# Kernel optimization log

Measured on AMD Instinct MI355X. Metric: run time of the kernel, lower is better.

The kernel has to match this reference:

```python
import jax, jax.numpy as jnp
import numpy as np

BATCH = 4096
IN_SIZES = [1024, 1024, 1024, 1024]
EMB = 2048  # embracement_size


def setup_inputs() -> dict:
    key = jax.random.key(0)
    keys = jax.random.split(key, 3 * len(IN_SIZES))
    inp = {}
    for i, d in enumerate(IN_SIZES):
        inp[f"x{i}"] = jax.random.normal(keys[3 * i], (BATCH, d), dtype=jnp.float32)
        # Linear params (Kaiming-ish scale)
        inp[f"W{i}"] = jax.random.normal(keys[3 * i + 1], (d, EMB), dtype=jnp.float32) / np.sqrt(d)
        inp[f"b{i}"] = jax.random.normal(keys[3 * i + 2], (EMB,), dtype=jnp.float32) * 0.01
    return inp


def _sample_indices(batch, num_feats, emb):
    # availabilities=None, selection_probabilities=None -> uniform p over modalities
    # multinomial(p, num_samples=emb, replacement=True) == categorical over log p
    logits = jnp.zeros((batch, num_feats), dtype=jnp.float32)  # uniform
    k = jax.random.key(42)
    # shape (emb, batch) broadcasts against logits batch shape (batch,)
    idx = jax.random.categorical(k, logits, axis=-1, shape=(emb, batch))
    return idx.T  # [batch, emb]


def reference(x0, W0, b0, x1, W1, b1, x2, W2, b2, x3, W3, b3):
    xs = [x0, x1, x2, x3]
    Ws = [W0, W1, W2, W3]
    bs = [b0, b1, b2, b3]
    # docking: Linear + ReLU per modality -> [batch, EMB, num_feats]
    dock = jnp.stack([jax.nn.relu(x @ W + b) for x, W, b in zip(xs, Ws, bs)], axis=-1)
    B, E, F = dock.shape
    idx = _sample_indices(B, F, E)  # [B, E] int32
    # gather along modality axis (replaces one-hot multiply-sum)
    out = jnp.take_along_axis(dock, idx[:, :, None], axis=-1)[..., 0]
    return out  # [batch, EMB]
```

## Files before the change

kernel.cpp:

```cpp
#include <hip/hip_runtime.h>
#include <stdint.h>


typedef short short8 __attribute__((ext_vector_type(8)));
typedef float floatx4 __attribute__((ext_vector_type(4)));

#define B_DIM 4096
#define K_DIM 1024
#define E_DIM 2048

__device__ __forceinline__ uint32_t rotl32(uint32_t x, uint32_t r) {
  return __builtin_amdgcn_alignbit(x, x, 32u - r);
}

__device__ __forceinline__ uint16_t f2bf(float x) {
  uint32_t u = __float_as_uint(x);
  u += 0x7FFFu + ((u >> 16) & 1u);
  return (uint16_t)(u >> 16);
}

__device__ __forceinline__ void threefry(uint32_t x0, uint32_t x1,
                                         uint32_t& o0, uint32_t& o1) {
  const uint32_t ks0 = 0u;
  const uint32_t ks1 = 42u;
  const uint32_t ks2 = 0x1BD11BDAu ^ 42u;
  x0 += ks0; x1 += ks1;
#define TF_R(r) { x0 += x1; x1 = rotl32(x1, r); x1 ^= x0; }
  TF_R(13) TF_R(15) TF_R(26) TF_R(6)
  x0 += ks1; x1 += ks2 + 1u;
  TF_R(17) TF_R(29) TF_R(16) TF_R(24)
  x0 += ks2; x1 += ks0 + 2u;
  TF_R(13) TF_R(15) TF_R(26) TF_R(6)
  x0 += ks0; x1 += ks1 + 3u;
  TF_R(17) TF_R(29) TF_R(16) TF_R(24)
  x0 += ks1; x1 += ks2 + 4u;
  TF_R(13) TF_R(15) TF_R(26) TF_R(6)
  x0 += ks2; x1 += ks0 + 5u;
#undef TF_R
  o0 = x0; o1 = x1;
}

__global__ __launch_bounds__(256) void prep_kernel(
    const float* __restrict__ x0, const float* __restrict__ x1,
    const float* __restrict__ x2, const float* __restrict__ x3,
    const float* __restrict__ W0, const float* __restrict__ W1,
    const float* __restrict__ W2, const float* __restrict__ W3,
    uint16_t* __restrict__ xb, uint16_t* __restrict__ Wt,
    uint8_t* __restrict__ idx1) {
  __shared__ float tile[32][33];
  const uint32_t g = blockIdx.x;
  const int t = threadIdx.x;
  const int f = g >> 11;
  const uint32_t ip = g & 2047u;

  const float* x = (f == 0) ? x0 : (f == 1) ? x1 : (f == 2) ? x2 : x3;
  const size_t xoff = ((size_t)ip * 256 + t) * 8;
  float4 v0 = *(const float4*)(x + xoff);
  float4 v1 = *(const float4*)(x + xoff + 4);

  const float* W = (f == 0) ? W0 : (f == 1) ? W1 : (f == 2) ? W2 : W3;
  const int e0 = (int)(ip & 63) * 32, k0 = (int)(ip >> 6) * 32;
  const int tx = t & 31, ty = t >> 5;
  float wv[4];
#pragma unroll
  for (int i = 0; i < 4; ++i)
    wv[i] = W[(size_t)(k0 + ty + i * 8) * E_DIM + e0 + tx];

  const uint32_t o0i = (g * 256u + t) * 4u;
  uint32_t byte = 0;
#pragma unroll
  for (uint32_t q = 0; q < 4; ++q) {
    uint32_t c = (o0i + q) << 2;
    uint32_t best = 0, bi = 0;
#pragma unroll
    for (uint32_t ff = 0; ff < 4; ++ff) {
      uint32_t y0, y1;
      threefry(0u, c + ff, y0, y1);
      uint32_t m = (y0 ^ y1) >> 9;
      if (ff == 0) best = m;
      else if (m > best) { best = m; bi = ff; }
    }
    byte |= bi << (2 * q);
  }
  idx1[g * 256u + t] = (uint8_t)byte;

  {
    union { uint16_t h[8]; uint64_t q[2]; } p;
    p.h[0] = f2bf(v0.x); p.h[1] = f2bf(v0.y);
    p.h[2] = f2bf(v0.z); p.h[3] = f2bf(v0.w);
    p.h[4] = f2bf(v1.x); p.h[5] = f2bf(v1.y);
    p.h[6] = f2bf(v1.z); p.h[7] = f2bf(v1.w);
    uint64_t* dst = (uint64_t*)(xb + (size_t)f * B_DIM * K_DIM + xoff);
    dst[0] = p.q[0]; dst[1] = p.q[1];
  }

#pragma unroll
  for (int i = 0; i < 4; ++i) tile[ty + i * 8][tx] = wv[i];
  __syncthreads();
  {
    const int el = t >> 3, kc = (t & 7) * 4;
    union { uint16_t h[4]; uint64_t q; } p;
#pragma unroll
    for (int i = 0; i < 4; ++i) p.h[i] = f2bf(tile[kc + i][el]);
    uint16_t* dst = Wt + (size_t)f * E_DIM * K_DIM;
    *(uint64_t*)(dst + (size_t)(e0 + el) * K_DIM + k0 + kc) = p.q;
  }
}

__device__ __forceinline__ void async16(const uint16_t* g, uint16_t* lds) {
  __builtin_amdgcn_global_load_lds(
      (const __attribute__((address_space(1))) void*)g,
      (__attribute__((address_space(3))) void*)lds, 16, 0, 0);
}

__global__ __launch_bounds__(256, 2) void gemm_fused(
    const uint16_t* __restrict__ Ab, const uint16_t* __restrict__ Bbt,
    const uint32_t* __restrict__ idx2,
    const float* __restrict__ bias0, const float* __restrict__ bias1,
    const float* __restrict__ bias2, const float* __restrict__ bias3,
    float* __restrict__ out) {
  __shared__ uint16_t As[2][128 * 64];
  __shared__ uint16_t Bs[2][128 * 64];

  const int tid = threadIdx.x;
  const int w = tid >> 6;
  const int l = tid & 63;
  const int mBase = blockIdx.y * 128;
  const int nBase = blockIdx.x * 128;

  const int wm = (w >> 1) * 64, wn = (w & 1) * 64;
  const int sr = l >> 3;
  const int skc = ((l & 7) ^ sr) * 8;
  const int fr = l & 15, fq = l >> 4;

  const int b_hi0 = (mBase + wm) >> 4;
  uint32_t iw[4][4];
#pragma unroll
  for (int ni = 0; ni < 4; ++ni) {
    int col = nBase + wn + ni * 16 + fr;
#pragma unroll
    for (int mi = 0; mi < 4; ++mi)
      iw[ni][mi] = idx2[(size_t)col * (B_DIM / 16) + b_hi0 + mi];
  }

  floatx4 res[4][4] = {};

#pragma unroll 1
  for (int f = 0; f < 4; ++f) {
    const uint16_t* A = Ab  + (size_t)f * B_DIM * K_DIM + (size_t)mBase * K_DIM;
    const uint16_t* B = Bbt + (size_t)f * E_DIM * K_DIM + (size_t)nBase * K_DIM;
    const uint16_t* Aw = A + (size_t)(32 * w + sr) * K_DIM + skc;
    const uint16_t* Bw = B + (size_t)(32 * w + sr) * K_DIM + skc;

    floatx4 acc[4][4] = {};

#pragma unroll
    for (int tt = 0; tt < 4; ++tt) {
      async16(Aw + (size_t)(8 * tt) * K_DIM, &As[0][(4 * w + tt) * 512]);
      async16(Bw + (size_t)(8 * tt) * K_DIM, &Bs[0][(4 * w + tt) * 512]);
    }
    __syncthreads();

    int buf = 0;
#pragma unroll 1
    for (int kt = 0; kt < 16; ++kt) {
      int kn = (kt + 1) * 64;
      if (kt + 1 < 16) {
#pragma unroll
        for (int tt = 0; tt < 4; ++tt) {
          async16(Aw + (size_t)(8 * tt) * K_DIM + kn, &As[buf ^ 1][(4 * w + tt) * 512]);
          async16(Bw + (size_t)(8 * tt) * K_DIM + kn, &Bs[buf ^ 1][(4 * w + tt) * 512]);
        }
      }
#pragma unroll
      for (int h = 0; h < 2; ++h) {
        short8 a[4], b[4];
        const int ch = h * 4 + fq;
#pragma unroll
        for (int mi = 0; mi < 4; ++mi) {
          int row = wm + mi * 16 + fr;
          a[mi] = *(const short8*)&As[buf][row * 64 + (ch ^ (fr & 7)) * 8];
        }
#pragma unroll
        for (int ni = 0; ni < 4; ++ni) {
          int row = wn + ni * 16 + fr;
          b[ni] = *(const short8*)&Bs[buf][row * 64 + (ch ^ (fr & 7)) * 8];
        }
#pragma unroll
        for (int mi = 0; mi < 4; ++mi)
#pragma unroll
          for (int ni = 0; ni < 4; ++ni)
            acc[mi][ni] = __builtin_amdgcn_mfma_f32_16x16x32_bf16(
                a[mi], b[ni], acc[mi][ni], 0, 0, 0);
      }
      __syncthreads();
      buf ^= 1;
    }

    const float* bias = (f == 0) ? bias0 : (f == 1) ? bias1
                      : (f == 2) ? bias2 : bias3;
#pragma unroll
    for (int ni = 0; ni < 4; ++ni) {
      float bvf = bias[nBase + wn + ni * 16 + fr];
#pragma unroll
      for (int mi = 0; mi < 4; ++mi) {
        uint32_t wd = iw[ni][mi];
#pragma unroll
        for (int r = 0; r < 4; ++r) {
          uint32_t sel = (wd >> (2 * (fq * 4 + r))) & 3u;
          if (sel == (uint32_t)f) res[mi][ni][r] = acc[mi][ni][r] + bvf;
        }
      }
    }
  }

#pragma unroll
  for (int ni = 0; ni < 4; ++ni) {
    int col = nBase + wn + ni * 16 + fr;
#pragma unroll
    for (int mi = 0; mi < 4; ++mi) {
      int row0 = mBase + wm + mi * 16 + fq * 4;
#pragma unroll
      for (int r = 0; r < 4; ++r) {
        float o = res[mi][ni][r];
        __builtin_nontemporal_store(o > 0.f ? o : 0.f,
                                    &out[(size_t)(row0 + r) * E_DIM + col]);
      }
    }
  }
}

extern "C" void kernel_launch(void* const* d_in, const int* in_sizes, int n_in,
                              void* d_out, int out_size, void* d_ws, size_t ws_size,
                              hipStream_t stream) {
  const float* x[4]; const float* W[4]; const float* bs[4];
  for (int f = 0; f < 4; ++f) {
    x[f]  = (const float*)d_in[3 * f + 0];
    W[f]  = (const float*)d_in[3 * f + 1];
    bs[f] = (const float*)d_in[3 * f + 2];
  }
  char* ws = (char*)d_ws;
  uint16_t* xb  = (uint16_t*)ws;
  uint16_t* Wt  = (uint16_t*)(ws + (size_t)32 * 1024 * 1024);
  uint8_t*  idx1 = (uint8_t*)(ws + (size_t)48 * 1024 * 1024);
  float* out = (float*)d_out;

  prep_kernel<<<dim3(8192), dim3(256), 0, stream>>>(
      x[0], x[1], x[2], x[3], W[0], W[1], W[2], W[3], xb, Wt, idx1);
  gemm_fused<<<dim3(E_DIM / 128, B_DIM / 128), dim3(256), 0, stream>>>(
      xb, Wt, (const uint32_t*)idx1, bs[0], bs[1], bs[2], bs[3], out);
}
```

Before: 254.1 us.

## Use 256x128 tiles with 8 waves, triple-buffered pipeline across modalities

The GEMM block grows to 256x128 with 512 threads (8 waves) and a grid-swizzled tile mapping. The four per-modality K loops are flattened into one 64-step loop with a 3-stage LDS ring, explicit vmcnt waits and raw barriers, so prefetch continues across modality boundaries. Biases are preloaded into registers and MFMA sections get raised wave priority. The aim is better operand reuse, fewer pipeline drains and L2 locality, at the cost of 144KB of LDS per block, which may limit occupancy to one block per CU despite launch_bounds(512,2).

```diff
diff --git a/kernel.cpp b/kernel.cpp
--- a/kernel.cpp
+++ b/kernel.cpp
@@ -113,25 +113,35 @@
       (__attribute__((address_space(3))) void*)lds, 16, 0, 0);
 }
 
-__global__ __launch_bounds__(256, 2) void gemm_fused(
+#define PLANE_A ((size_t)B_DIM * K_DIM)
+#define PLANE_B ((size_t)E_DIM * K_DIM)
+
+__global__ __launch_bounds__(512, 2) void gemm_fused(
     const uint16_t* __restrict__ Ab, const uint16_t* __restrict__ Bbt,
     const uint32_t* __restrict__ idx2,
     const float* __restrict__ bias0, const float* __restrict__ bias1,
     const float* __restrict__ bias2, const float* __restrict__ bias3,
     float* __restrict__ out) {
-  __shared__ uint16_t As[2][128 * 64];
-  __shared__ uint16_t Bs[2][128 * 64];
+  __shared__ uint16_t As[3][256 * 64];
+  __shared__ uint16_t Bs[3][128 * 64];
 
   const int tid = threadIdx.x;
   const int w = tid >> 6;
   const int l = tid & 63;
-  const int mBase = blockIdx.y * 128;
-  const int nBase = blockIdx.x * 128;
-
-  const int wm = (w >> 1) * 64, wn = (w & 1) * 64;
+
+  const int flat = (int)(blockIdx.y * gridDim.x + blockIdx.x);
+  const int swz = (flat & 7) * 32 + (flat >> 3);
+  const int mBase = (swz >> 4) * 256;
+  const int nBase = (swz & 15) * 128;
+
+  const int wm = (w >> 1) * 64;
+  const int wn = (w & 1) * 64;
+  const int fr = l & 15, fq = l >> 4;
+
   const int sr = l >> 3;
-  const int skc = ((l & 7) ^ sr) * 8;
-  const int fr = l & 15, fq = l >> 4;
+  const int sgk = ((l & 7) ^ sr) * 8;
+  const uint16_t* aBase = Ab + (size_t)(mBase + 32 * w + sr) * K_DIM + sgk;
+  const uint16_t* bBase = Bbt + (size_t)(nBase + 16 * w + sr) * K_DIM + sgk;
 
   const int b_hi0 = (mBase + wm) >> 4;
   uint32_t iw[4][4];
@@ -142,76 +152,91 @@
     for (int mi = 0; mi < 4; ++mi)
       iw[ni][mi] = idx2[(size_t)col * (B_DIM / 16) + b_hi0 + mi];
   }
-
+  float bz0[4], bz1[4], bz2[4], bz3[4];
+#pragma unroll
+  for (int ni = 0; ni < 4; ++ni) {
+    int col = nBase + wn + ni * 16 + fr;
+    bz0[ni] = bias0[col]; bz1[ni] = bias1[col];
+    bz2[ni] = bias2[col]; bz3[ni] = bias3[col];
+  }
+
+  auto stage = [&](int t, int tb) {
+    const int fA = t >> 4, ko = (t & 15) * 64;
+    const uint16_t* pA = aBase + (size_t)fA * PLANE_A + ko;
+    const uint16_t* pB = bBase + (size_t)fA * PLANE_B + ko;
+#pragma unroll
+    for (int tt = 0; tt < 4; ++tt)
+      async16(pA + (size_t)(8 * tt) * K_DIM, &As[tb][(4 * w + tt) * 512]);
+#pragma unroll
+    for (int tt = 0; tt < 2; ++tt)
+      async16(pB + (size_t)(8 * tt) * K_DIM, &Bs[tb][(2 * w + tt) * 512]);
+  };
+
+  floatx4 acc[4][4] = {};
   floatx4 res[4][4] = {};
 
+  stage(0, 0);
+  stage(1, 1);
+  asm volatile("s_waitcnt vmcnt(6)" ::: "memory");
+  __builtin_amdgcn_s_barrier();
+  asm volatile("" ::: "memory");
+
+  int cb = 0, tb = 2;
 #pragma unroll 1
-  for (int f = 0; f < 4; ++f) {
-    const uint16_t* A = Ab  + (size_t)f * B_DIM * K_DIM + (size_t)mBase * K_DIM;
-    const uint16_t* B = Bbt + (size_t)f * E_DIM * K_DIM + (size_t)nBase * K_DIM;
-    const uint16_t* Aw = A + (size_t)(32 * w + sr) * K_DIM + skc;
-    const uint16_t* Bw = B + (size_t)(32 * w + sr) * K_DIM + skc;
-
-    floatx4 acc[4][4] = {};
-
-#pragma unroll
-    for (int tt = 0; tt < 4; ++tt) {
-      async16(Aw + (size_t)(8 * tt) * K_DIM, &As[0][(4 * w + tt) * 512]);
-      async16(Bw + (size_t)(8 * tt) * K_DIM, &Bs[0][(4 * w + tt) * 512]);
-    }
-    __syncthreads();
-
-    int buf = 0;
-#pragma unroll 1
-    for (int kt = 0; kt < 16; ++kt) {
-      int kn = (kt + 1) * 64;
-      if (kt + 1 < 16) {
-#pragma unroll
-        for (int tt = 0; tt < 4; ++tt) {
-          async16(Aw + (size_t)(8 * tt) * K_DIM + kn, &As[buf ^ 1][(4 * w + tt) * 512]);
-          async16(Bw + (size_t)(8 * tt) * K_DIM + kn, &Bs[buf ^ 1][(4 * w + tt) * 512]);
+  for (int kt = 0; kt < 64; ++kt) {
+    if (kt + 2 < 64) stage(kt + 2, tb);
+
+#pragma unroll
+    for (int h = 0; h < 2; ++h) {
+      short8 a[4], b[4];
+      const int ch = h * 4 + fq;
+      const int kc = (ch ^ (fr & 7)) * 8;
+#pragma unroll
+      for (int mi = 0; mi < 4; ++mi)
+        a[mi] = *(const short8*)&As[cb][(wm + mi * 16 + fr) * 64 + kc];
+#pragma unroll
+      for (int ni = 0; ni < 4; ++ni)
+        b[ni] = *(const short8*)&Bs[cb][(wn + ni * 16 + fr) * 64 + kc];
+      __builtin_amdgcn_s_setprio(1);
+#pragma unroll
+      for (int mi = 0; mi < 4; ++mi)
+#pragma unroll
+        for (int ni = 0; ni < 4; ++ni)
+          acc[mi][ni] = __builtin_amdgcn_mfma_f32_16x16x32_bf16(
+              a[mi], b[ni], acc[mi][ni], 0, 0, 0);
+      __builtin_amdgcn_s_setprio(0);
+    }
+
+    if ((kt & 15) == 15) {
+      const int f = kt >> 4;
+#pragma unroll
+      for (int ni = 0; ni < 4; ++ni) {
+        float bv = (f == 0) ? bz0[ni] : (f == 1) ? bz1[ni]
+                 : (f == 2) ? bz2[ni] : bz3[ni];
+#pragma unroll
+        for (int mi = 0; mi < 4; ++mi) {
+          uint32_t wd = iw[ni][mi];
+#pragma unroll
+          for (int r = 0; r < 4; ++r) {
+            uint32_t sel = (wd >> (2 * (fq * 4 + r))) & 3u;
+            if (sel == (uint32_t)f) res[mi][ni][r] = acc[mi][ni][r] + bv;
+            acc[mi][ni][r] = 0.f;
+          }
         }
       }
-#pragma unroll
-      for (int h = 0; h < 2; ++h) {
-        short8 a[4], b[4];
-        const int ch = h * 4 + fq;
-#pragma unroll
-        for (int mi = 0; mi < 4; ++mi) {
-          int row = wm + mi * 16 + fr;
-          a[mi] = *(const short8*)&As[buf][row * 64 + (ch ^ (fr & 7)) * 8];
-        }
-#pragma unroll
-        for (int ni = 0; ni < 4; ++ni) {
-          int row = wn + ni * 16 + fr;
-          b[ni] = *(const short8*)&Bs[buf][row * 64 + (ch ^ (fr & 7)) * 8];
-        }
-#pragma unroll
-        for (int mi = 0; mi < 4; ++mi)
-#pragma unroll
-          for (int ni = 0; ni < 4; ++ni)
-            acc[mi][ni] = __builtin_amdgcn_mfma_f32_16x16x32_bf16(
-                a[mi], b[ni], acc[mi][ni], 0, 0, 0);
-      }
-      __syncthreads();
-      buf ^= 1;
-    }
-
-    const float* bias = (f == 0) ? bias0 : (f == 1) ? bias1
-                      : (f == 2) ? bias2 : bias3;
-#pragma unroll
-    for (int ni = 0; ni < 4; ++ni) {
-      float bvf = bias[nBase + wn + ni * 16 + fr];
-#pragma unroll
-      for (int mi = 0; mi < 4; ++mi) {
-        uint32_t wd = iw[ni][mi];
-#pragma unroll
-        for (int r = 0; r < 4; ++r) {
-          uint32_t sel = (wd >> (2 * (fq * 4 + r))) & 3u;
-          if (sel == (uint32_t)f) res[mi][ni][r] = acc[mi][ni][r] + bvf;
-        }
-      }
-    }
+    }
+
+    if (kt < 62) {
+      asm volatile("s_waitcnt vmcnt(6)" ::: "memory");
+      __builtin_amdgcn_s_barrier();
+      asm volatile("" ::: "memory");
+    } else if (kt < 63) {
+      asm volatile("s_waitcnt vmcnt(0)" ::: "memory");
+      __builtin_amdgcn_s_barrier();
+      asm volatile("" ::: "memory");
+    }
+    cb = (cb == 2) ? 0 : cb + 1;
+    tb = (tb == 2) ? 0 : tb + 1;
   }
 
 #pragma unroll
@@ -247,6 +272,6 @@
 
   prep_kernel<<<dim3(8192), dim3(256), 0, stream>>>(
       x[0], x[1], x[2], x[3], W[0], W[1], W[2], W[3], xb, Wt, idx1);
-  gemm_fused<<<dim3(E_DIM / 128, B_DIM / 128), dim3(256), 0, stream>>>(
+  gemm_fused<<<dim3(E_DIM / 128, B_DIM / 256), dim3(512), 0, stream>>>(
       xb, Wt, (const uint32_t*)idx1, bs[0], bs[1], bs[2], bs[3], out);
 }
```

New measurement: 274.4 us. 1.08x slower.
